# Kernel tuning notes

Measured on AMD Instinct MI355X. Metric: run time of the kernel, lower is better.

The kernel has to match this reference:

```python
import jax, jax.numpy as jnp
import numpy as np

VAR0, VAR1 = 0.1, 0.2          # SSD variances
IOU_THRESH = 0.5
NUM_CLASSES = 21
NEGPOS_RATIO = 3
ALPHA = 1.0


def mid_to_corner(b):
    # [cx,cy,w,h] -> [xmin,ymin,xmax,ymax]
    return jnp.concatenate([b[:, :2] - b[:, 2:] / 2, b[:, :2] + b[:, 2:] / 2], axis=1)


def jaccard(box_a, box_b):
    # box_a [n,4], box_b [P,4] corner form -> IoU [n,P]
    lt = jnp.maximum(box_a[:, None, :2], box_b[None, :, :2])
    rb = jnp.minimum(box_a[:, None, 2:], box_b[None, :, 2:])
    wh = jnp.clip(rb - lt, 0.0)
    inter = wh[..., 0] * wh[..., 1]
    area_a = (box_a[:, 2] - box_a[:, 0]) * (box_a[:, 3] - box_a[:, 1])
    area_b = (box_b[:, 2] - box_b[:, 0]) * (box_b[:, 3] - box_b[:, 1])
    union = area_a[:, None] + area_b[None, :] - inter
    return inter / union


def encode_offset(matched, priors):
    # matched corner form [P,4], priors center form [P,4]
    g_cxcy = ((matched[:, :2] + matched[:, 2:]) / 2 - priors[:, :2]) / (VAR0 * priors[:, 2:])
    g_wh = jnp.log((matched[:, 2:] - matched[:, :2]) / priors[:, 2:]) / VAR1
    return jnp.concatenate([g_cxcy, g_wh], axis=1)


def match_one(gt_box, gt_cls, valid, priors_corner, priors_mid):
    # gt_box [n,4], gt_cls [n], valid [n] bool; priors [P,4]
    n = gt_box.shape[0]
    P = priors_corner.shape[0]
    ovl = jaccard(gt_box, priors_corner)                    # [n,P]
    ovl = jnp.where(valid[:, None], ovl, -1.0)              # mask padded GTs
    best_truth_idx = jnp.argmax(ovl, axis=0)                # [P]
    best_truth_ovl = jnp.max(ovl, axis=0)                   # [P]
    best_prior_idx = jnp.argmax(ovl, axis=1)                # [n]
    bpi = jnp.where(valid, best_prior_idx, P)               # OOB for padded -> dropped
    best_truth_ovl = best_truth_ovl.at[bpi].set(2.0, mode='drop')
    best_truth_idx = best_truth_idx.at[bpi].set(jnp.arange(n), mode='drop')
    matches = gt_box[best_truth_idx]                        # [P,4]
    loc = encode_offset(matches, priors_mid)                # [P,4]
    conf = gt_cls[best_truth_idx].astype(jnp.int32) + 1     # [P]
    conf = jnp.where(best_truth_ovl < IOU_THRESH, 0, conf)
    return loc, conf


def setup_inputs() -> dict:
    key = jax.random.key(0)
    k = jax.random.split(key, 8)
    B, P, C, NMAX = 64, 8732, 21, 50
    confidence = jax.random.normal(k[0], (B, P, C), dtype=jnp.float32)
    location = 0.1 * jax.random.normal(k[1], (B, P, 4), dtype=jnp.float32)
    cxcy = jax.random.uniform(k[2], (P, 2), minval=0.05, maxval=0.95)
    pwh = jax.random.uniform(k[3], (P, 2), minval=0.05, maxval=0.4)
    prior_boxes = jnp.concatenate([cxcy, pwh], axis=1).astype(jnp.float32)
    xymin = jax.random.uniform(k[4], (B, NMAX, 2), minval=0.0, maxval=0.6)
    gwh = jax.random.uniform(k[5], (B, NMAX, 2), minval=0.05, maxval=0.35)
    cls = jax.random.randint(k[6], (B, NMAX), 0, C - 1).astype(jnp.float32)
    labels = jnp.concatenate([xymin, xymin + gwh, cls[..., None]], axis=-1).astype(jnp.float32)
    obj_count = jax.random.randint(k[7], (B, 1), 1, NMAX + 1).astype(jnp.int32)
    return {"confidence": confidence, "location": location,
            "prior_boxes": prior_boxes, "labels": labels, "obj_count": obj_count}


def reference(confidence, location, prior_boxes, labels, obj_count):
    B, P, C = confidence.shape
    NMAX = labels.shape[1]
    priors_corner = mid_to_corner(prior_boxes)
    valid = jnp.arange(NMAX)[None, :] < obj_count            # [B,NMAX]
    loc_t, conf_t = jax.vmap(match_one, in_axes=(0, 0, 0, None, None))(
        labels[..., :4], labels[..., 4], valid, priors_corner, prior_boxes)
    # loc_t [B,P,4] float, conf_t [B,P] int32

    pos = conf_t > 0                                          # [B,P]
    # smooth-L1 over positive anchors (sum reduction)
    d = jnp.abs(location - loc_t)
    sl1 = jnp.where(d < 1.0, 0.5 * d * d, d - 0.5)
    loss_loc = jnp.sum(sl1 * pos[..., None].astype(sl1.dtype))

    # hard negative mining score: global-max logsumexp minus target logit
    bc = confidence.reshape(-1, C)
    x_max = jnp.max(bc)
    lse = jnp.log(jnp.sum(jnp.exp(bc - x_max), axis=1)) + x_max
    tgt_logit = jnp.take_along_axis(bc, conf_t.reshape(-1, 1), axis=1)[:, 0]
    loss_c = (lse - tgt_logit).reshape(B, P)
    loss_c = jnp.where(pos, 0.0, loss_c)
    loss_idx = jnp.argsort(-loss_c, axis=1)                   # descending sort
    idx_rank = jnp.argsort(loss_idx, axis=1)
    num_pos = jnp.sum(pos.astype(jnp.int32), axis=1, keepdims=True)   # [B,1]
    num_neg = jnp.clip(NEGPOS_RATIO * num_pos, None, P - 1)
    neg = idx_rank < num_neg                                  # [B,P]

    # standard cross entropy over selected (pos|neg) anchors, sum reduction
    logp = jax.nn.log_softmax(confidence, axis=-1)            # [B,P,C]
    nll = -jnp.take_along_axis(logp, conf_t[..., None], axis=-1)[..., 0]
    sel = jnp.logical_or(pos, neg)
    loss_conf = jnp.sum(nll * sel.astype(nll.dtype))

    N = jnp.sum(num_pos).astype(confidence.dtype)
    return (ALPHA * loss_loc / N, loss_conf / N)
```

## Files before the change

kernel.cpp:

```cpp
#include <hip/hip_runtime.h>
#include <math.h>

#define Bn 64
#define Pn 8732
#define Cn 21
#define NMAXn 50
#define PX 35

__global__ __launch_bounds__(256) void k_matchbp(const float* __restrict__ labels,
                                                 const int* __restrict__ objc,
                                                 const float* __restrict__ priors,
                                                 int* __restrict__ match,
                                                 int* __restrict__ bp) {
    const int bx = blockIdx.x;
    const int tid = threadIdx.x;
    __shared__ float lab[NMAXn * 5];
    __shared__ int cnt_s;
    __shared__ float sv[256];
    __shared__ int si[256];

    if (bx < Bn * PX) {
        const int b = bx / PX;
        const int p = (bx % PX) * 256 + tid;
        for (int i = tid; i < NMAXn * 5; i += 256) lab[i] = labels[b * NMAXn * 5 + i];
        if (tid == 0) cnt_s = objc[b];
        __syncthreads();
        if (p >= Pn) return;
        const float4 pr = reinterpret_cast<const float4*>(priors)[p];
        const float px0 = pr.x - 0.5f * pr.z, py0 = pr.y - 0.5f * pr.w;
        const float px1 = pr.x + 0.5f * pr.z, py1 = pr.y + 0.5f * pr.w;
        const float parea = (px1 - px0) * (py1 - py0);
        const int cnt = cnt_s;
        float best = -1.0f;
        int bidx = 0;
        for (int n = 0; n < cnt; ++n) {
            const float gx0 = lab[n * 5 + 0], gy0 = lab[n * 5 + 1];
            const float gx1 = lab[n * 5 + 2], gy1 = lab[n * 5 + 3];
            const float lx = fmaxf(gx0, px0), ly = fmaxf(gy0, py0);
            const float rx = fminf(gx1, px1), ry = fminf(gy1, py1);
            const float w = fmaxf(rx - lx, 0.0f), h = fmaxf(ry - ly, 0.0f);
            const float inter = w * h;
            const float ga = (gx1 - gx0) * (gy1 - gy0);
            const float v = inter / (ga + parea - inter);
            if (v > best) { best = v; bidx = n; }
        }
        match[(size_t)b * Pn + p] = (bidx << 1) | (best >= 0.5f ? 1 : 0);
    } else {
        const int idx = bx - Bn * PX;
        const int b = idx / NMAXn;
        const int n = idx % NMAXn;
        if (n >= objc[b]) return;
        const float gx0 = labels[(b * NMAXn + n) * 5 + 0];
        const float gy0 = labels[(b * NMAXn + n) * 5 + 1];
        const float gx1 = labels[(b * NMAXn + n) * 5 + 2];
        const float gy1 = labels[(b * NMAXn + n) * 5 + 3];
        const float ga = (gx1 - gx0) * (gy1 - gy0);
        float best = -1.0f;
        int bidx = 0;
        for (int p = tid; p < Pn; p += 256) {
            const float4 pr = reinterpret_cast<const float4*>(priors)[p];
            const float px0 = pr.x - 0.5f * pr.z, py0 = pr.y - 0.5f * pr.w;
            const float px1 = pr.x + 0.5f * pr.z, py1 = pr.y + 0.5f * pr.w;
            const float lx = fmaxf(gx0, px0), ly = fmaxf(gy0, py0);
            const float rx = fminf(gx1, px1), ry = fminf(gy1, py1);
            const float w = fmaxf(rx - lx, 0.0f), h = fmaxf(ry - ly, 0.0f);
            const float inter = w * h;
            const float pa = (px1 - px0) * (py1 - py0);
            const float v = inter / (ga + pa - inter);
            if (v > best) { best = v; bidx = p; }
        }
        sv[tid] = best;
        si[tid] = bidx;
        __syncthreads();
        for (int s = 128; s > 0; s >>= 1) {
            if (tid < s) {
                const float ov = sv[tid + s];
                const int oi = si[tid + s];
                if (ov > sv[tid] || (ov == sv[tid] && oi < si[tid])) {
                    sv[tid] = ov;
                    si[tid] = oi;
                }
            }
            __syncthreads();
        }
        if (tid == 0) bp[b * NMAXn + n] = si[0];
    }
}

__global__ __launch_bounds__(256) void k_main(const float* __restrict__ conf,
                                              const float* __restrict__ loc,
                                              const float* __restrict__ priors,
                                              const float* __restrict__ labels,
                                              const int* __restrict__ objc,
                                              const int* __restrict__ match,
                                              const int* __restrict__ bp,
                                              float* __restrict__ lc,
                                              float* __restrict__ part_loc,
                                              float* __restrict__ part_nll,
                                              int* __restrict__ part_np,
                                              int* __restrict__ done) {
    const int b = blockIdx.y;
    const int px = blockIdx.x;
    const int p0 = px * 256;
    const int tid = threadIdx.x;
    const int rows = min(256, Pn - p0);
    const int p = p0 + ((tid < rows) ? tid : 0);
    const size_t gi = (size_t)b * Pn + p;
    const int w = match[gi];

    if (b == 0 && px == 0 && tid == 0) *done = 0;

    __shared__ float sconf[256 * Cn];
    __shared__ float lab[NMAXn * 5];
    __shared__ int sbp[NMAXn];
    const float4* src = reinterpret_cast<const float4*>(conf + ((size_t)b * Pn + p0) * Cn);
    const int n4 = rows * Cn / 4;
    for (int i = tid; i < n4; i += 256) reinterpret_cast<float4*>(sconf)[i] = src[i];
    for (int i = tid; i < NMAXn * 5; i += 256) lab[i] = labels[b * NMAXn * 5 + i];
    if (tid < NMAXn) sbp[tid] = (tid < objc[b]) ? bp[b * NMAXn + tid] : -1;
    __syncthreads();

    float my_loc = 0.0f, my_nll = 0.0f;
    int my_np = 0;
    if (tid < rows) {
        int ti = w >> 1;
        int fl = w & 1;
#pragma unroll
        for (int n = 0; n < NMAXn; ++n) {
            if (sbp[n] == p) { ti = n; fl = 1; }
        }
        const int ct = fl ? ((int)lab[ti * 5 + 4] + 1) : 0;
        const float* row = sconf + tid * Cn;
        float m = row[0];
#pragma unroll
        for (int j = 1; j < Cn; ++j) m = fmaxf(m, row[j]);
        float s2 = 0.0f;
#pragma unroll
        for (int j = 0; j < Cn; ++j) s2 += __expf(row[j] - m);
        const float nll = __logf(s2) + m - row[ct];
        if (ct > 0) {
            lc[gi] = 0.0f;
            my_np = 1;
            my_nll = nll;
            const float4 pr = reinterpret_cast<const float4*>(priors)[p];
            const float gx0 = lab[ti * 5 + 0], gy0 = lab[ti * 5 + 1];
            const float gx1 = lab[ti * 5 + 2], gy1 = lab[ti * 5 + 3];
            const float tx = ((gx0 + gx1) * 0.5f - pr.x) / (0.1f * pr.z);
            const float ty = ((gy0 + gy1) * 0.5f - pr.y) / (0.1f * pr.w);
            const float tw = __logf((gx1 - gx0) / pr.z) * 5.0f;
            const float th = __logf((gy1 - gy0) / pr.w) * 5.0f;
            const float4 l = reinterpret_cast<const float4*>(loc)[gi];
            float d;
            d = fabsf(l.x - tx); my_loc += (d < 1.0f) ? 0.5f * d * d : d - 0.5f;
            d = fabsf(l.y - ty); my_loc += (d < 1.0f) ? 0.5f * d * d : d - 0.5f;
            d = fabsf(l.z - tw); my_loc += (d < 1.0f) ? 0.5f * d * d : d - 0.5f;
            d = fabsf(l.w - th); my_loc += (d < 1.0f) ? 0.5f * d * d : d - 0.5f;
        } else {
            lc[gi] = nll;
        }
    }
    for (int off = 32; off > 0; off >>= 1) {
        my_loc += __shfl_down(my_loc, off);
        my_nll += __shfl_down(my_nll, off);
        my_np += __shfl_down(my_np, off);
    }
    __shared__ float rl[4], rn[4];
    __shared__ int rp[4];
    const int wid = tid >> 6, lane = tid & 63;
    if (lane == 0) { rl[wid] = my_loc; rn[wid] = my_nll; rp[wid] = my_np; }
    __syncthreads();
    if (tid == 0) {
        const int g = b * PX + px;
        part_loc[g] = rl[0] + rl[1] + rl[2] + rl[3];
        part_nll[g] = rn[0] + rn[1] + rn[2] + rn[3];
        part_np[g] = rp[0] + rp[1] + rp[2] + rp[3];
    }
}

__global__ __launch_bounds__(512) void k_neg(const float* __restrict__ lc,
                                             const float* __restrict__ part_loc,
                                             const float* __restrict__ part_nll,
                                             const int* __restrict__ part_np,
                                             float* __restrict__ negsum,
                                             int* __restrict__ done,
                                             float* __restrict__ out) {
    const int b = blockIdx.x;
    const int tid = threadIdx.x;
    __shared__ float s[Pn];
    __shared__ int cslot[32];
    __shared__ int np_sh;
    __shared__ float redf[8], redf2[8];
    __shared__ int redc[8];
    __shared__ int islast;

    const float4* src = reinterpret_cast<const float4*>(lc + (size_t)b * Pn);
    for (int i = tid; i < Pn / 4; i += 512) reinterpret_cast<float4*>(s)[i] = src[i];
    if (tid < 32) cslot[tid] = 0;
    if (tid < 64) {
        int npl = (tid < PX) ? part_np[b * PX + tid] : 0;
        for (int off = 32; off > 0; off >>= 1) npl += __shfl_down(npl, off);
        if (tid == 0) np_sh = npl;
    }
    __syncthreads();
    const int k = min(3 * np_sh, Pn - 1);
    const int wid = tid >> 6, lane = tid & 63;

    unsigned lo = 0u, hi = 0x7F800000u;
#pragma unroll 1
    for (int it = 0; it < 31; ++it) {
        const unsigned mid = lo + ((hi - lo) >> 1);
        const float fm = __uint_as_float(mid);
        int c = 0;
        for (int i = tid; i < Pn / 4; i += 512) {
            const float4 v = reinterpret_cast<const float4*>(s)[i];
            c += (v.x >= fm) + (v.y >= fm) + (v.z >= fm) + (v.w >= fm);
        }
        for (int off = 32; off > 0; off >>= 1) c += __shfl_down(c, off);
        if (lane == 0) atomicAdd(&cslot[it], c);
        __syncthreads();
        const int tot = cslot[it];
        if (tot >= k) lo = mid;
        else hi = mid;
    }
    const float v = __uint_as_float(lo);

    float sm = 0.0f;
    int c = 0;
    for (int i = tid; i < Pn / 4; i += 512) {
        const float4 q = reinterpret_cast<const float4*>(s)[i];
        if (q.x > v) { sm += q.x; ++c; }
        if (q.y > v) { sm += q.y; ++c; }
        if (q.z > v) { sm += q.z; ++c; }
        if (q.w > v) { sm += q.w; ++c; }
    }
    for (int off = 32; off > 0; off >>= 1) {
        sm += __shfl_down(sm, off);
        c += __shfl_down(c, off);
    }
    if (lane == 0) { redf[wid] = sm; redc[wid] = c; }
    __syncthreads();
    if (tid == 0) {
        float st = 0.0f;
        int ct = 0;
#pragma unroll
        for (int i = 0; i < 8; ++i) { st += redf[i]; ct += redc[i]; }
        negsum[b] = st + (float)(k - ct) * v;
        __threadfence();
        islast = (atomicAdd(done, 1) == Bn - 1) ? 1 : 0;
    }
    __syncthreads();
    if (!islast) return;
    __threadfence();

    float sl = 0.0f, sn = 0.0f;
    int np = 0;
    for (int i = tid; i < Bn * PX; i += 512) {
        sl += part_loc[i];
        sn += part_nll[i];
        np += part_np[i];
    }
    if (tid < Bn) sn += negsum[tid];
    for (int off = 32; off > 0; off >>= 1) {
        sl += __shfl_down(sl, off);
        sn += __shfl_down(sn, off);
        np += __shfl_down(np, off);
    }
    if (lane == 0) { redf[wid] = sn; redf2[wid] = sl; redc[wid] = np; }
    __syncthreads();
    if (tid == 0) {
        float tsl = 0.0f, tsn = 0.0f;
        int tnp = 0;
#pragma unroll
        for (int i = 0; i < 8; ++i) { tsl += redf2[i]; tsn += redf[i]; tnp += redc[i]; }
        const float fN = (float)tnp;
        out[0] = tsl / fN;
        out[1] = tsn / fN;
    }
}

extern "C" void kernel_launch(void* const* d_in, const int* in_sizes, int n_in,
                              void* d_out, int out_size, void* d_ws, size_t ws_size,
                              hipStream_t stream) {
    const float* conf = (const float*)d_in[0];
    const float* loc = (const float*)d_in[1];
    const float* priors = (const float*)d_in[2];
    const float* labels = (const float*)d_in[3];
    const int* objc = (const int*)d_in[4];
    float* out = (float*)d_out;

    float* part_loc = (float*)d_ws;
    float* part_nll = part_loc + Bn * PX;
    int* part_np = (int*)(part_nll + Bn * PX);
    float* negsum = (float*)(part_np + Bn * PX);
    int* bp = (int*)(negsum + Bn);
    int* match = bp + Bn * NMAXn;
    float* lc = (float*)(match + (size_t)Bn * Pn);
    int* done = (int*)(lc + (size_t)Bn * Pn);

    k_matchbp<<<Bn * PX + Bn * NMAXn, 256, 0, stream>>>(labels, objc, priors, match, bp);
    dim3 g(PX, Bn);
    k_main<<<g, 256, 0, stream>>>(conf, loc, priors, labels, objc, match, bp, lc,
                                  part_loc, part_nll, part_np, done);
    k_neg<<<Bn, 512, 0, stream>>>(lc, part_loc, part_nll, part_np, negsum, done, out);
}
```

Measured before the change: 79.65 us.

## Fuse per-prior matching into main kernel and restructure best-prior and negative kernels

Per-prior GT matching moves from the first kernel into k_main, which removes the intermediate match buffer write and read. Best-prior search becomes one 1024-thread block per image. Each block caches corner-form priors in LDS and reduces with wave shuffles instead of a shared-memory tree. k_neg is widened to 1024 threads and replaces its per-iteration LDS atomics with double-buffered per-wave partial counts. The trade-off is that the best-prior kernel now runs only 64 blocks, each looping serially over its GTs, which may leave most CUs idle.

After: 180.7 us. +126.9%, slower.

```diff
diff --git a/kernel.cpp b/kernel.cpp
--- a/kernel.cpp
+++ b/kernel.cpp
@@ -6,84 +6,61 @@
 #define Cn 21
 #define NMAXn 50
 #define PX 35
-
-__global__ __launch_bounds__(256) void k_matchbp(const float* __restrict__ labels,
-                                                 const int* __restrict__ objc,
-                                                 const float* __restrict__ priors,
-                                                 int* __restrict__ match,
-                                                 int* __restrict__ bp) {
-    const int bx = blockIdx.x;
+#define Wn 16
+
+__global__ __launch_bounds__(1024) void k_bp(const float* __restrict__ labels,
+                                             const int* __restrict__ objc,
+                                             const float* __restrict__ priors,
+                                             int* __restrict__ bp) {
+    const int b = blockIdx.x;
     const int tid = threadIdx.x;
+    const int lane = tid & 63, wid = tid >> 6;
+    __shared__ float4 pc[Pn];
     __shared__ float lab[NMAXn * 5];
-    __shared__ int cnt_s;
-    __shared__ float sv[256];
-    __shared__ int si[256];
-
-    if (bx < Bn * PX) {
-        const int b = bx / PX;
-        const int p = (bx % PX) * 256 + tid;
-        for (int i = tid; i < NMAXn * 5; i += 256) lab[i] = labels[b * NMAXn * 5 + i];
-        if (tid == 0) cnt_s = objc[b];
-        __syncthreads();
-        if (p >= Pn) return;
+    __shared__ float wv[NMAXn][Wn];
+    __shared__ int wi[NMAXn][Wn];
+    const int cnt = objc[b];
+    for (int p = tid; p < Pn; p += 1024) {
         const float4 pr = reinterpret_cast<const float4*>(priors)[p];
-        const float px0 = pr.x - 0.5f * pr.z, py0 = pr.y - 0.5f * pr.w;
-        const float px1 = pr.x + 0.5f * pr.z, py1 = pr.y + 0.5f * pr.w;
-        const float parea = (px1 - px0) * (py1 - py0);
-        const int cnt = cnt_s;
-        float best = -1.0f;
-        int bidx = 0;
-        for (int n = 0; n < cnt; ++n) {
-            const float gx0 = lab[n * 5 + 0], gy0 = lab[n * 5 + 1];
-            const float gx1 = lab[n * 5 + 2], gy1 = lab[n * 5 + 3];
-            const float lx = fmaxf(gx0, px0), ly = fmaxf(gy0, py0);
-            const float rx = fminf(gx1, px1), ry = fminf(gy1, py1);
-            const float w = fmaxf(rx - lx, 0.0f), h = fmaxf(ry - ly, 0.0f);
-            const float inter = w * h;
-            const float ga = (gx1 - gx0) * (gy1 - gy0);
-            const float v = inter / (ga + parea - inter);
-            if (v > best) { best = v; bidx = n; }
-        }
-        match[(size_t)b * Pn + p] = (bidx << 1) | (best >= 0.5f ? 1 : 0);
-    } else {
-        const int idx = bx - Bn * PX;
-        const int b = idx / NMAXn;
-        const int n = idx % NMAXn;
-        if (n >= objc[b]) return;
-        const float gx0 = labels[(b * NMAXn + n) * 5 + 0];
-        const float gy0 = labels[(b * NMAXn + n) * 5 + 1];
-        const float gx1 = labels[(b * NMAXn + n) * 5 + 2];
-        const float gy1 = labels[(b * NMAXn + n) * 5 + 3];
+        pc[p] = make_float4(pr.x - 0.5f * pr.z, pr.y - 0.5f * pr.w,
+                            pr.x + 0.5f * pr.z, pr.y + 0.5f * pr.w);
+    }
+    for (int i = tid; i < NMAXn * 5; i += 1024) lab[i] = labels[b * NMAXn * 5 + i];
+    __syncthreads();
+    for (int n = 0; n < cnt; ++n) {
+        const float gx0 = lab[n * 5 + 0], gy0 = lab[n * 5 + 1];
+        const float gx1 = lab[n * 5 + 2], gy1 = lab[n * 5 + 3];
         const float ga = (gx1 - gx0) * (gy1 - gy0);
         float best = -1.0f;
         int bidx = 0;
-        for (int p = tid; p < Pn; p += 256) {
-            const float4 pr = reinterpret_cast<const float4*>(priors)[p];
-            const float px0 = pr.x - 0.5f * pr.z, py0 = pr.y - 0.5f * pr.w;
-            const float px1 = pr.x + 0.5f * pr.z, py1 = pr.y + 0.5f * pr.w;
-            const float lx = fmaxf(gx0, px0), ly = fmaxf(gy0, py0);
-            const float rx = fminf(gx1, px1), ry = fminf(gy1, py1);
+        for (int p = tid; p < Pn; p += 1024) {
+            const float4 c = pc[p];
+            const float lx = fmaxf(gx0, c.x), ly = fmaxf(gy0, c.y);
+            const float rx = fminf(gx1, c.z), ry = fminf(gy1, c.w);
             const float w = fmaxf(rx - lx, 0.0f), h = fmaxf(ry - ly, 0.0f);
             const float inter = w * h;
-            const float pa = (px1 - px0) * (py1 - py0);
+            const float pa = (c.z - c.x) * (c.w - c.y);
             const float v = inter / (ga + pa - inter);
             if (v > best) { best = v; bidx = p; }
         }
-        sv[tid] = best;
-        si[tid] = bidx;
-        __syncthreads();
-        for (int s = 128; s > 0; s >>= 1) {
-            if (tid < s) {
-                const float ov = sv[tid + s];
-                const int oi = si[tid + s];
-                if (ov > sv[tid] || (ov == sv[tid] && oi < si[tid])) {
-                    sv[tid] = ov;
-                    si[tid] = oi;
-                }
-            }
-            __syncthreads();
-        }
-        if (tid == 0) bp[b * NMAXn + n] = si[0];
+        for (int off = 32; off > 0; off >>= 1) {
+            const float ov = __shfl_down(best, off);
+            const int oi = __shfl_down(bidx, off);
+            if (ov > best || (ov == best && oi < bidx)) { best = ov; bidx = oi; }
+        }
+        if (lane == 0) { wv[n][wid] = best; wi[n][wid] = bidx; }
+    }
+    __syncthreads();
+    if (tid < cnt) {
+        float best = wv[tid][0];
+        int bidx = wi[tid][0];
+#pragma unroll
+        for (int w = 1; w < Wn; ++w) {
+            const float ov = wv[tid][w];
+            const int oi = wi[tid][w];
+            if (ov > best || (ov == best && oi < bidx)) { best = ov; bidx = oi; }
+        }
+        bp[b * NMAXn + tid] = bidx;
     }
 }
 
@@ -92,7 +69,6 @@
                                               const float* __restrict__ priors,
                                               const float* __restrict__ labels,
                                               const int* __restrict__ objc,
-                                              const int* __restrict__ match,
                                               const int* __restrict__ bp,
                                               float* __restrict__ lc,
                                               float* __restrict__ part_loc,
@@ -106,29 +82,45 @@
     const int rows = min(256, Pn - p0);
     const int p = p0 + ((tid < rows) ? tid : 0);
     const size_t gi = (size_t)b * Pn + p;
-    const int w = match[gi];
 
     if (b == 0 && px == 0 && tid == 0) *done = 0;
 
     __shared__ float sconf[256 * Cn];
     __shared__ float lab[NMAXn * 5];
     __shared__ int sbp[NMAXn];
+    __shared__ int cnt_s;
     const float4* src = reinterpret_cast<const float4*>(conf + ((size_t)b * Pn + p0) * Cn);
     const int n4 = rows * Cn / 4;
     for (int i = tid; i < n4; i += 256) reinterpret_cast<float4*>(sconf)[i] = src[i];
     for (int i = tid; i < NMAXn * 5; i += 256) lab[i] = labels[b * NMAXn * 5 + i];
-    if (tid < NMAXn) sbp[tid] = (tid < objc[b]) ? bp[b * NMAXn + tid] : -1;
+    if (tid < NMAXn) sbp[tid] = bp[b * NMAXn + tid];
+    if (tid == 0) cnt_s = objc[b];
     __syncthreads();
 
     float my_loc = 0.0f, my_nll = 0.0f;
     int my_np = 0;
     if (tid < rows) {
-        int ti = w >> 1;
-        int fl = w & 1;
-#pragma unroll
-        for (int n = 0; n < NMAXn; ++n) {
-            if (sbp[n] == p) { ti = n; fl = 1; }
-        }
+        const int cnt = cnt_s;
+        const float4 pr = reinterpret_cast<const float4*>(priors)[p];
+        const float px0 = pr.x - 0.5f * pr.z, py0 = pr.y - 0.5f * pr.w;
+        const float px1 = pr.x + 0.5f * pr.z, py1 = pr.y + 0.5f * pr.w;
+        const float parea = (px1 - px0) * (py1 - py0);
+        float best = -1.0f;
+        int bidx = 0, fidx = -1;
+        for (int n = 0; n < cnt; ++n) {
+            const float gx0 = lab[n * 5 + 0], gy0 = lab[n * 5 + 1];
+            const float gx1 = lab[n * 5 + 2], gy1 = lab[n * 5 + 3];
+            const float lx = fmaxf(gx0, px0), ly = fmaxf(gy0, py0);
+            const float rx = fminf(gx1, px1), ry = fminf(gy1, py1);
+            const float w = fmaxf(rx - lx, 0.0f), h = fmaxf(ry - ly, 0.0f);
+            const float inter = w * h;
+            const float ga = (gx1 - gx0) * (gy1 - gy0);
+            const float v = inter / (ga + parea - inter);
+            if (v > best) { best = v; bidx = n; }
+            if (sbp[n] == p) fidx = n;
+        }
+        const int ti = (fidx >= 0) ? fidx : bidx;
+        const int fl = (fidx >= 0) || (best >= 0.5f);
         const int ct = fl ? ((int)lab[ti * 5 + 4] + 1) : 0;
         const float* row = sconf + tid * Cn;
         float m = row[0];
@@ -142,7 +134,6 @@
             lc[gi] = 0.0f;
             my_np = 1;
             my_nll = nll;
-            const float4 pr = reinterpret_cast<const float4*>(priors)[p];
             const float gx0 = lab[ti * 5 + 0], gy0 = lab[ti * 5 + 1];
             const float gx1 = lab[ti * 5 + 2], gy1 = lab[ti * 5 + 3];
             const float tx = ((gx0 + gx1) * 0.5f - pr.x) / (0.1f * pr.z);
@@ -177,25 +168,24 @@
     }
 }
 
-__global__ __launch_bounds__(512) void k_neg(const float* __restrict__ lc,
-                                             const float* __restrict__ part_loc,
-                                             const float* __restrict__ part_nll,
-                                             const int* __restrict__ part_np,
-                                             float* __restrict__ negsum,
-                                             int* __restrict__ done,
-                                             float* __restrict__ out) {
+__global__ __launch_bounds__(1024) void k_neg(const float* __restrict__ lc,
+                                              const float* __restrict__ part_loc,
+                                              const float* __restrict__ part_nll,
+                                              const int* __restrict__ part_np,
+                                              float* __restrict__ negsum,
+                                              int* __restrict__ done,
+                                              float* __restrict__ out) {
     const int b = blockIdx.x;
     const int tid = threadIdx.x;
+    const int lane = tid & 63, wid = tid >> 6;
     __shared__ float s[Pn];
-    __shared__ int cslot[32];
-    __shared__ int np_sh;
-    __shared__ float redf[8], redf2[8];
-    __shared__ int redc[8];
-    __shared__ int islast;
+    __shared__ int redc[2][Wn];
+    __shared__ float redf[Wn], redf2[Wn];
+    __shared__ int redi[Wn];
+    __shared__ int np_sh, islast;
 
     const float4* src = reinterpret_cast<const float4*>(lc + (size_t)b * Pn);
-    for (int i = tid; i < Pn / 4; i += 512) reinterpret_cast<float4*>(s)[i] = src[i];
-    if (tid < 32) cslot[tid] = 0;
+    for (int i = tid; i < Pn / 4; i += 1024) reinterpret_cast<float4*>(s)[i] = src[i];
     if (tid < 64) {
         int npl = (tid < PX) ? part_np[b * PX + tid] : 0;
         for (int off = 32; off > 0; off >>= 1) npl += __shfl_down(npl, off);
@@ -203,7 +193,6 @@
     }
     __syncthreads();
     const int k = min(3 * np_sh, Pn - 1);
-    const int wid = tid >> 6, lane = tid & 63;
 
     unsigned lo = 0u, hi = 0x7F800000u;
 #pragma unroll 1
@@ -211,14 +200,16 @@
         const unsigned mid = lo + ((hi - lo) >> 1);
         const float fm = __uint_as_float(mid);
         int c = 0;
-        for (int i = tid; i < Pn / 4; i += 512) {
+        for (int i = tid; i < Pn / 4; i += 1024) {
             const float4 v = reinterpret_cast<const float4*>(s)[i];
             c += (v.x >= fm) + (v.y >= fm) + (v.z >= fm) + (v.w >= fm);
         }
         for (int off = 32; off > 0; off >>= 1) c += __shfl_down(c, off);
-        if (lane == 0) atomicAdd(&cslot[it], c);
+        if (lane == 0) redc[it & 1][wid] = c;
         __syncthreads();
-        const int tot = cslot[it];
+        int tot = 0;
+#pragma unroll
+        for (int w = 0; w < Wn; ++w) tot += redc[it & 1][w];
         if (tot >= k) lo = mid;
         else hi = mid;
     }
@@ -226,7 +217,7 @@
 
     float sm = 0.0f;
     int c = 0;
-    for (int i = tid; i < Pn / 4; i += 512) {
+    for (int i = tid; i < Pn / 4; i += 1024) {
         const float4 q = reinterpret_cast<const float4*>(s)[i];
         if (q.x > v) { sm += q.x; ++c; }
         if (q.y > v) { sm += q.y; ++c; }
@@ -237,13 +228,13 @@
         sm += __shfl_down(sm, off);
         c += __shfl_down(c, off);
     }
-    if (lane == 0) { redf[wid] = sm; redc[wid] = c; }
+    if (lane == 0) { redf[wid] = sm; redi[wid] = c; }
     __syncthreads();
     if (tid == 0) {
         float st = 0.0f;
         int ct = 0;
 #pragma unroll
-        for (int i = 0; i < 8; ++i) { st += redf[i]; ct += redc[i]; }
+        for (int w = 0; w < Wn; ++w) { st += redf[w]; ct += redi[w]; }
         negsum[b] = st + (float)(k - ct) * v;
         __threadfence();
         islast = (atomicAdd(done, 1) == Bn - 1) ? 1 : 0;
@@ -254,7 +245,7 @@
 
     float sl = 0.0f, sn = 0.0f;
     int np = 0;
-    for (int i = tid; i < Bn * PX; i += 512) {
+    for (int i = tid; i < Bn * PX; i += 1024) {
         sl += part_loc[i];
         sn += part_nll[i];
         np += part_np[i];
@@ -265,13 +256,13 @@
         sn += __shfl_down(sn, off);
         np += __shfl_down(np, off);
     }
-    if (lane == 0) { redf[wid] = sn; redf2[wid] = sl; redc[wid] = np; }
+    if (lane == 0) { redf[wid] = sn; redf2[wid] = sl; redi[wid] = np; }
     __syncthreads();
     if (tid == 0) {
         float tsl = 0.0f, tsn = 0.0f;
         int tnp = 0;
 #pragma unroll
-        for (int i = 0; i < 8; ++i) { tsl += redf2[i]; tsn += redf[i]; tnp += redc[i]; }
+        for (int w = 0; w < Wn; ++w) { tsl += redf2[w]; tsn += redf[w]; tnp += redi[w]; }
         const float fN = (float)tnp;
         out[0] = tsl / fN;
         out[1] = tsn / fN;
@@ -293,13 +284,12 @@
     int* part_np = (int*)(part_nll + Bn * PX);
     float* negsum = (float*)(part_np + Bn * PX);
     int* bp = (int*)(negsum + Bn);
-    int* match = bp + Bn * NMAXn;
-    float* lc = (float*)(match + (size_t)Bn * Pn);
+    float* lc = (float*)(bp + Bn * NMAXn);
     int* done = (int*)(lc + (size_t)Bn * Pn);
 
-    k_matchbp<<<Bn * PX + Bn * NMAXn, 256, 0, stream>>>(labels, objc, priors, match, bp);
+    k_bp<<<Bn, 1024, 0, stream>>>(labels, objc, priors, bp);
     dim3 g(PX, Bn);
-    k_main<<<g, 256, 0, stream>>>(conf, loc, priors, labels, objc, match, bp, lc,
+    k_main<<<g, 256, 0, stream>>>(conf, loc, priors, labels, objc, bp, lc,
                                   part_loc, part_nll, part_np, done);
-    k_neg<<<Bn, 512, 0, stream>>>(lc, part_loc, part_nll, part_np, negsum, done, out);
-}
+    k_neg<<<Bn, 1024, 0, stream>>>(lc, part_loc, part_nll, part_np, negsum, done, out);
+}
```
